# Optimization experiments

Measured on AMD Instinct MI355X. Metric: run time of the kernel, lower is better.

The kernel has to match this reference:

```python
import jax, jax.numpy as jnp
import numpy as np

SIGMA = 0.2
BN_EPS = 1e-5


def setup_inputs() -> dict:
    key = jax.random.key(0)
    k1, k2, k3, k4 = jax.random.split(key, 4)
    B, F, K, M = 8, 16384, 3, 64
    normals = jax.random.normal(k1, (B, 3, F), dtype=jnp.float32)
    # normalize to unit vectors (face normals), keeps math well-conditioned
    normals = normals / jnp.linalg.norm(normals, axis=1, keepdims=True)
    weight_alpha = jax.random.uniform(k2, (1, M, 4), dtype=jnp.float32) * np.pi
    weight_beta = jax.random.uniform(k3, (1, M, 4), dtype=jnp.float32) * 2 * np.pi
    bn_gamma = jnp.ones((M,), dtype=jnp.float32)
    bn_beta = jnp.zeros((M,), dtype=jnp.float32)
    neighbor_index = jax.random.randint(k4, (B, F, K), 0, F, dtype=jnp.int64)
    return {"normals": normals, "weight_alpha": weight_alpha,
            "weight_beta": weight_beta, "bn_gamma": bn_gamma,
            "bn_beta": bn_beta, "neighbor_index": neighbor_index}


def reference(normals, weight_alpha, weight_beta, bn_gamma, bn_beta, neighbor_index):
    # normals: [B, 3, F]; neighbor_index: [B, F, K]
    B, _, F = normals.shape
    K = neighbor_index.shape[-1]
    # kernel points on unit sphere from spherical angles: [3, M, 4]
    sa, ca = jnp.sin(weight_alpha), jnp.cos(weight_alpha)
    sb, cb = jnp.sin(weight_beta), jnp.cos(weight_beta)
    w = jnp.concatenate([sa * cb, sa * sb, ca], axis=0)  # [3, M, 4]

    nt = jnp.transpose(normals, (0, 2, 1))  # [B, F, 3]
    # gather neighbor normals per batch: [B, F, K, 3]
    neigh = jax.vmap(lambda n, idx: n[idx])(nt, neighbor_index)
    # points per face: center + K neighbors -> [B, F, K+1, 3]
    pts = jnp.concatenate([nt[:, :, None, :], neigh], axis=2)

    # squared distance via expansion: ||p||^2 + ||w||^2 - 2 p.w
    dot = jnp.einsum('bfic,cmj->bmfij', pts, w)        # [B, M, F, K+1, 4]
    p2 = jnp.sum(pts * pts, axis=-1)                   # [B, F, K+1]
    w2 = jnp.sum(w * w, axis=0)                        # [M, 4]
    dist = (p2[:, None, :, :, None] + w2[None, :, None, None, :] - 2.0 * dot)

    feat = jnp.sum(jnp.exp(dist / (-2.0 * SIGMA ** 2)), axis=(3, 4))
    feat = feat / float((K + 1) * 4)                   # [B, M, F]

    # BatchNorm1d (training-mode batch stats over B and F per channel M)
    mean = jnp.mean(feat, axis=(0, 2), keepdims=True)
    var = jnp.var(feat, axis=(0, 2), keepdims=True)
    xhat = (feat - mean) / jnp.sqrt(var + BN_EPS)
    out = xhat * bn_gamma[None, :, None] + bn_beta[None, :, None]
    return jax.nn.relu(out)
```

## Files before the change

kernel.cpp:

```cpp
#include <hip/hip_runtime.h>
#include <hip/hip_fp16.h>

#define B_DIM 8
#define F_DIM 16384
#define K_DIM 3
#define M_DIM 64
#define LOG2E 1.4426950408889634f

#define WS_Q   65536
#define WS_G   131072
#define WS_NEED ((size_t)WS_G * 4 + (size_t)B_DIM * F_DIM * M_DIM * 2)

#define FB_WS_Q 32768

__global__ __launch_bounds__(256) void fkc_g16_kernel(
    const float* __restrict__ normals,
    const float* __restrict__ walpha,
    const float* __restrict__ wbeta,
    __half* __restrict__ G)
{
    __shared__ float4 sW[256];
    const int tid = threadIdx.x;
    {
        float a = walpha[tid], b = wbeta[tid];
        float sa = sinf(a), ca = cosf(a);
        float sb = sinf(b), cb = cosf(b);
        float wx = sa * cb, wy = sa * sb, wz = ca;
        float w2 = wx * wx + wy * wy + wz * wz;
        sW[tid] = make_float4(wx * 25.0f * LOG2E, wy * 25.0f * LOG2E,
                              wz * 25.0f * LOG2E, -12.5f * LOG2E * (w2 + 1.0f));
    }
    __syncthreads();

    const int b  = blockIdx.x >> 8;
    const int fc = blockIdx.x & 255;
    const int fl = tid & 63, mq = tid >> 6;
    const int f  = (fc << 6) + fl;

    const float* nb = normals + (size_t)b * 3 * F_DIM;
    const float px = nb[f], py = nb[F_DIM + f], pz = nb[2 * F_DIM + f];

    union { __half2 h2[8]; float4 f4[2]; } u;
#pragma unroll
    for (int r = 0; r < 8; ++r) {
        float g[2];
#pragma unroll
        for (int c = 0; c < 2; ++c) {
            const int m = mq * 16 + r * 2 + c;
            float4 w0 = sW[m * 4 + 0], w1 = sW[m * 4 + 1];
            float4 w2 = sW[m * 4 + 2], w3 = sW[m * 4 + 3];
            float e0 = __builtin_amdgcn_exp2f(fmaf(w0.x, px, fmaf(w0.y, py, fmaf(w0.z, pz, w0.w))));
            float e1 = __builtin_amdgcn_exp2f(fmaf(w1.x, px, fmaf(w1.y, py, fmaf(w1.z, pz, w1.w))));
            float e2 = __builtin_amdgcn_exp2f(fmaf(w2.x, px, fmaf(w2.y, py, fmaf(w2.z, pz, w2.w))));
            float e3 = __builtin_amdgcn_exp2f(fmaf(w3.x, px, fmaf(w3.y, py, fmaf(w3.z, pz, w3.w))));
            g[c] = (e0 + e1) + (e2 + e3);
        }
        u.h2[r] = __floats2half2_rn(g[0], g[1]);
    }
    float4* dst = (float4*)(G + ((size_t)(b * F_DIM + f)) * M_DIM + mq * 16);
    dst[0] = u.f4[0];
    dst[1] = u.f4[1];
}

__global__ __launch_bounds__(256) void fkc_gath16_kernel(
    const __half* __restrict__ G,
    const int*   __restrict__ nidx,
    float* __restrict__ out,
    float* __restrict__ ws)
{
    __shared__ float T[2][128][34];
    const int tid = threadIdx.x;
    const int b  = blockIdx.x & 7;
    const int fc = blockIdx.x >> 3;
    const int fl = tid & 127, mh = tid >> 7;
    const int f  = (fc << 7) + fl;

    const int* ib = nidx + ((size_t)(b * F_DIM + f)) * K_DIM;
    const int i1 = ib[0], i2 = ib[1], i3 = ib[2];

    const size_t gb = (size_t)b * F_DIM * M_DIM + (size_t)mh * 32;
    const float4* r0 = (const float4*)(G + gb + (size_t)f  * M_DIM);
    const float4* r1 = (const float4*)(G + gb + (size_t)i1 * M_DIM);
    const float4* r2 = (const float4*)(G + gb + (size_t)i2 * M_DIM);
    const float4* r3 = (const float4*)(G + gb + (size_t)i3 * M_DIM);

    union F4H { float4 f4; __half2 h2[4]; };
    float v[32];
#pragma unroll
    for (int c = 0; c < 4; ++c) {
        F4H a, x, y, z, acc;
        a.f4 = r0[c]; x.f4 = r1[c]; y.f4 = r2[c]; z.f4 = r3[c];
#pragma unroll
        for (int k = 0; k < 4; ++k) {
            acc.h2[k] = __hadd2(__hadd2(a.h2[k], x.h2[k]), __hadd2(y.h2[k], z.h2[k]));
            float2 t = __half22float2(acc.h2[k]);
            v[c * 8 + k * 2]     = t.x;
            v[c * 8 + k * 2 + 1] = t.y;
        }
    }

    {
        float* ob = out + ((size_t)b * M_DIM + mh * 32) * F_DIM + f;
#pragma unroll
        for (int k = 0; k < 32; ++k) ob[(size_t)k * F_DIM] = v[k];
    }

#pragma unroll
    for (int k = 0; k < 32; ++k) T[mh][fl][k] = v[k];
    __syncthreads();
    {
        const int rmh = tid >> 7, rml = (tid >> 2) & 31, rfs = tid & 3;
        float s = 0.f, q = 0.f;
#pragma unroll
        for (int i = 0; i < 32; ++i) {
            float val = T[rmh][rfs * 32 + i][rml];
            s += val;
            q = fmaf(val, val, q);
        }
        s += __shfl_xor(s, 1, 64);  q += __shfl_xor(q, 1, 64);
        s += __shfl_xor(s, 2, 64);  q += __shfl_xor(q, 2, 64);
        if (rfs == 0) {
            int m = rmh * 32 + rml;
            int slot = m * 1024 + b * 128 + fc;
            ws[slot] = s;
            ws[WS_Q + slot] = q;
        }
    }
}

__global__ __launch_bounds__(256) void fkc_bn2_kernel(
    float* __restrict__ out,
    const float* __restrict__ gamma,
    const float* __restrict__ beta,
    const float* __restrict__ ws)
{
    __shared__ float sS[4], sQ[4];
    __shared__ float sAC[2];
    const int row = blockIdx.x;
    const int m = row & 63;
    const int tid = threadIdx.x;
    const int wave = tid >> 6, lane = tid & 63;

    {
        const float* p = ws + m * 1024;
        const float* r = ws + WS_Q + m * 1024;
        float s = (p[tid] + p[tid + 256]) + (p[tid + 512] + p[tid + 768]);
        float q = (r[tid] + r[tid + 256]) + (r[tid + 512] + r[tid + 768]);
#pragma unroll
        for (int off = 32; off >= 1; off >>= 1) {
            s += __shfl_xor(s, off, 64);
            q += __shfl_xor(q, off, 64);
        }
        if (lane == 0) { sS[wave] = s; sQ[wave] = q; }
    }
    __syncthreads();
    if (tid == 0) {
        float s = (sS[0] + sS[1]) + (sS[2] + sS[3]);
        float q = (sQ[0] + sQ[1]) + (sQ[2] + sQ[3]);
        const float invcnt = 1.0f / (float)(B_DIM * F_DIM);
        float meanS = s * invcnt;
        float meanF = meanS * (1.0f / 16.0f);
        float ef2   = q * invcnt * (1.0f / 256.0f);
        float var   = ef2 - meanF * meanF;
        float inv   = rsqrtf(var + 1e-5f);
        float A = gamma[m] * inv;
        sAC[0] = A * (1.0f / 16.0f);
        sAC[1] = beta[m] - meanF * A;
    }
    __syncthreads();

    const float A = sAC[0], C = sAC[1];
    float4* p4 = (float4*)(out + (size_t)row * F_DIM);
#pragma unroll
    for (int i = 0; i < 16; ++i) {
        float4 v = p4[tid + i * 256];
        v.x = fmaxf(fmaf(v.x, A, C), 0.0f);
        v.y = fmaxf(fmaf(v.y, A, C), 0.0f);
        v.z = fmaxf(fmaf(v.z, A, C), 0.0f);
        v.w = fmaxf(fmaf(v.w, A, C), 0.0f);
        p4[tid + i * 256] = v;
    }
}

__global__ __launch_bounds__(256) void fb_feat_kernel(
    const float* __restrict__ normals, const float* __restrict__ walpha,
    const float* __restrict__ wbeta, const int* __restrict__ nidx,
    float* __restrict__ feat_out, float* __restrict__ ws)
{
    __shared__ float4 sW[64];
    __shared__ float sRS[16][32], sRQ[16][32];
    const int tid = threadIdx.x;
    const int b  = blockIdx.x >> 8;
    const int mc = (blockIdx.x >> 6) & 3;
    const int fc = blockIdx.x & 63;
    if (tid < 64) {
        int idx = mc * 64 + tid;
        float a = walpha[idx], bb = wbeta[idx];
        float sa = sinf(a), ca = cosf(a);
        float sb = sinf(bb), cb = cosf(bb);
        float wx = sa * cb, wy = sa * sb, wz = ca;
        float w2 = wx * wx + wy * wy + wz * wz;
        sW[tid] = make_float4(wx * 25.0f * LOG2E, wy * 25.0f * LOG2E,
                              wz * 25.0f * LOG2E, -12.5f * LOG2E * (w2 + 1.0f));
    }
    __syncthreads();
    const int f = (fc << 8) + tid;
    const float* nb = normals + (size_t)b * 3 * F_DIM;
    float px[4], py[4], pz[4];
    px[0] = nb[f]; py[0] = nb[F_DIM + f]; pz[0] = nb[2 * F_DIM + f];
    const int* ib = nidx + ((size_t)b * F_DIM + f) * K_DIM;
#pragma unroll
    for (int k = 0; k < K_DIM; ++k) {
        int id = ib[k];
        px[k + 1] = nb[id]; py[k + 1] = nb[F_DIM + id]; pz[k + 1] = nb[2 * F_DIM + id];
    }
    const int wave = tid >> 6, lane = tid & 63;
    float* outb = feat_out + ((size_t)b * M_DIM + mc * 16) * F_DIM + f;
#pragma unroll 2
    for (int m = 0; m < 16; ++m) {
        float s0 = 0.f, s1 = 0.f, s2 = 0.f, s3 = 0.f;
#pragma unroll
        for (int j = 0; j < 4; ++j) {
            float4 w = sW[m * 4 + j];
            s0 += __builtin_amdgcn_exp2f(fmaf(w.x, px[0], fmaf(w.y, py[0], fmaf(w.z, pz[0], w.w))));
            s1 += __builtin_amdgcn_exp2f(fmaf(w.x, px[1], fmaf(w.y, py[1], fmaf(w.z, pz[1], w.w))));
            s2 += __builtin_amdgcn_exp2f(fmaf(w.x, px[2], fmaf(w.y, py[2], fmaf(w.z, pz[2], w.w))));
            s3 += __builtin_amdgcn_exp2f(fmaf(w.x, px[3], fmaf(w.y, py[3], fmaf(w.z, pz[3], w.w))));
        }
        float fv = ((s0 + s1) + (s2 + s3)) * (1.0f / 16.0f);
        outb[(size_t)m * F_DIM] = fv;
        float s = fv, q = fv * fv;
        s += __shfl_xor(s, 8, 64);  q += __shfl_xor(q, 8, 64);
        s += __shfl_xor(s, 16, 64); q += __shfl_xor(q, 16, 64);
        s += __shfl_xor(s, 32, 64); q += __shfl_xor(q, 32, 64);
        if (lane < 8) { sRS[m][wave * 8 + lane] = s; sRQ[m][wave * 8 + lane] = q; }
    }
    __syncthreads();
    {
        const int m = tid >> 4, j = tid & 15;
        float s = sRS[m][j] + sRS[m][j + 16];
        float q = sRQ[m][j] + sRQ[m][j + 16];
        s += __shfl_xor(s, 1, 64);  q += __shfl_xor(q, 1, 64);
        s += __shfl_xor(s, 2, 64);  q += __shfl_xor(q, 2, 64);
        s += __shfl_xor(s, 4, 64);  q += __shfl_xor(q, 4, 64);
        s += __shfl_xor(s, 8, 64);  q += __shfl_xor(q, 8, 64);
        if (j == 0) {
            int slot = (mc * 16 + m) * 512 + b * 64 + fc;
            ws[slot] = s;
            ws[FB_WS_Q + slot] = q;
        }
    }
}

__global__ __launch_bounds__(256) void fb_bn_kernel(
    float* __restrict__ out, const float* __restrict__ gamma,
    const float* __restrict__ beta, const float* __restrict__ ws)
{
    __shared__ float sS[4], sQ[4];
    __shared__ float sAC[2];
    const int row = blockIdx.x;
    const int m = row & 63;
    const int tid = threadIdx.x;
    const int wave = tid >> 6, lane = tid & 63;
    {
        float s = ws[m * 512 + tid]           + ws[m * 512 + tid + 256];
        float q = ws[FB_WS_Q + m * 512 + tid] + ws[FB_WS_Q + m * 512 + tid + 256];
#pragma unroll
        for (int off = 32; off >= 1; off >>= 1) {
            s += __shfl_xor(s, off, 64);
            q += __shfl_xor(q, off, 64);
        }
        if (lane == 0) { sS[wave] = s; sQ[wave] = q; }
    }
    __syncthreads();
    if (tid == 0) {
        float s = (sS[0] + sS[1]) + (sS[2] + sS[3]);
        float q = (sQ[0] + sQ[1]) + (sQ[2] + sQ[3]);
        const float invcnt = 1.0f / (float)(B_DIM * F_DIM);
        float mean = s * invcnt;
        float var  = q * invcnt - mean * mean;
        float inv  = rsqrtf(var + 1e-5f);
        float A = gamma[m] * inv;
        sAC[0] = A;
        sAC[1] = beta[m] - mean * A;
    }
    __syncthreads();
    const float A = sAC[0], C = sAC[1];
    float4* p4 = (float4*)(out + (size_t)row * F_DIM);
#pragma unroll
    for (int i = 0; i < 16; ++i) {
        float4 v = p4[tid + i * 256];
        v.x = fmaxf(fmaf(v.x, A, C), 0.0f);
        v.y = fmaxf(fmaf(v.y, A, C), 0.0f);
        v.z = fmaxf(fmaf(v.z, A, C), 0.0f);
        v.w = fmaxf(fmaf(v.w, A, C), 0.0f);
        p4[tid + i * 256] = v;
    }
}

extern "C" void kernel_launch(void* const* d_in, const int* in_sizes, int n_in,
                              void* d_out, int out_size, void* d_ws, size_t ws_size,
                              hipStream_t stream)
{
    const float* normals = (const float*)d_in[0];
    const float* walpha  = (const float*)d_in[1];
    const float* wbeta   = (const float*)d_in[2];
    const float* gamma   = (const float*)d_in[3];
    const float* beta    = (const float*)d_in[4];
    const int*   nidx    = (const int*)d_in[5];
    float* out = (float*)d_out;
    float* ws  = (float*)d_ws;

    if (ws_size >= WS_NEED) {
        __half* G = (__half*)(ws + WS_G);
        hipLaunchKernelGGL(fkc_g16_kernel, dim3(2048), dim3(256), 0, stream,
                           normals, walpha, wbeta, G);
        hipLaunchKernelGGL(fkc_gath16_kernel, dim3(1024), dim3(256), 0, stream,
                           G, nidx, out, ws);
        hipLaunchKernelGGL(fkc_bn2_kernel, dim3(B_DIM * M_DIM), dim3(256), 0, stream,
                           out, gamma, beta, ws);
    } else {
        hipLaunchKernelGGL(fb_feat_kernel, dim3(2048), dim3(256), 0, stream,
                           normals, walpha, wbeta, nidx, out, ws);
        hipLaunchKernelGGL(fb_bn_kernel, dim3(B_DIM * M_DIM), dim3(256), 0, stream,
                           out, gamma, beta, ws);
    }
}
```

Before: 47.20 us.

## Stage G writes through LDS for coalesced stores; shrink gather LDS to half2

The G-producing kernel now stages each block's 64x64 half tile in shared memory and writes it back as contiguous float4 rows, so global stores are fully coalesced instead of strided per-thread row chunks. The gather kernel stores its per-face sums to a half2 LDS tile instead of float, halving shared memory use, adds a launch-bounds occupancy hint of 8 blocks, and streams output writes inside the load loop instead of holding 32 floats in registers. The cost is an extra LDS round trip and barrier in the first kernel and half-precision unpacking in the statistics reduction.

```diff
diff --git a/kernel.cpp b/kernel.cpp
--- a/kernel.cpp
+++ b/kernel.cpp
@@ -20,6 +20,7 @@
     __half* __restrict__ G)
 {
     __shared__ float4 sW[256];
+    __shared__ __half Gt[64][68];
     const int tid = threadIdx.x;
     {
         float a = walpha[tid], b = wbeta[tid];
@@ -40,7 +41,7 @@
     const float* nb = normals + (size_t)b * 3 * F_DIM;
     const float px = nb[f], py = nb[F_DIM + f], pz = nb[2 * F_DIM + f];
 
-    union { __half2 h2[8]; float4 f4[2]; } u;
+    union { __half2 h2[8]; float2 f2[4]; } u;
 #pragma unroll
     for (int r = 0; r < 8; ++r) {
         float g[2];
@@ -57,18 +58,30 @@
         }
         u.h2[r] = __floats2half2_rn(g[0], g[1]);
     }
-    float4* dst = (float4*)(G + ((size_t)(b * F_DIM + f)) * M_DIM + mq * 16);
-    dst[0] = u.f4[0];
-    dst[1] = u.f4[1];
-}
-
-__global__ __launch_bounds__(256) void fkc_gath16_kernel(
+#pragma unroll
+    for (int c = 0; c < 4; ++c)
+        *(float2*)&Gt[fl][mq * 16 + c * 4] = u.f2[c];
+    __syncthreads();
+
+    {
+        const int r = tid >> 2, c0 = (tid & 3) * 16;
+        float2 w0 = *(float2*)&Gt[r][c0 + 0];
+        float2 w1 = *(float2*)&Gt[r][c0 + 4];
+        float2 w2 = *(float2*)&Gt[r][c0 + 8];
+        float2 w3 = *(float2*)&Gt[r][c0 + 12];
+        float4* dst = (float4*)(G + ((size_t)b * F_DIM + (fc << 6)) * M_DIM);
+        dst[tid * 2 + 0] = make_float4(w0.x, w0.y, w1.x, w1.y);
+        dst[tid * 2 + 1] = make_float4(w2.x, w2.y, w3.x, w3.y);
+    }
+}
+
+__global__ __launch_bounds__(256, 8) void fkc_gath16_kernel(
     const __half* __restrict__ G,
     const int*   __restrict__ nidx,
     float* __restrict__ out,
     float* __restrict__ ws)
 {
-    __shared__ float T[2][128][34];
+    __shared__ __half2 T2[2][128][18];
     const int tid = threadIdx.x;
     const int b  = blockIdx.x & 7;
     const int fc = blockIdx.x >> 3;
@@ -85,35 +98,31 @@
     const float4* r3 = (const float4*)(G + gb + (size_t)i3 * M_DIM);
 
     union F4H { float4 f4; __half2 h2[4]; };
-    float v[32];
+    float* ob = out + ((size_t)b * M_DIM + mh * 32) * F_DIM + f;
 #pragma unroll
     for (int c = 0; c < 4; ++c) {
-        F4H a, x, y, z, acc;
+        F4H a, x, y, z;
         a.f4 = r0[c]; x.f4 = r1[c]; y.f4 = r2[c]; z.f4 = r3[c];
+        union { __half2 h2[4]; float2 f2[2]; } hh;
 #pragma unroll
         for (int k = 0; k < 4; ++k) {
-            acc.h2[k] = __hadd2(__hadd2(a.h2[k], x.h2[k]), __hadd2(y.h2[k], z.h2[k]));
-            float2 t = __half22float2(acc.h2[k]);
-            v[c * 8 + k * 2]     = t.x;
-            v[c * 8 + k * 2 + 1] = t.y;
-        }
-    }
-
-    {
-        float* ob = out + ((size_t)b * M_DIM + mh * 32) * F_DIM + f;
-#pragma unroll
-        for (int k = 0; k < 32; ++k) ob[(size_t)k * F_DIM] = v[k];
-    }
-
-#pragma unroll
-    for (int k = 0; k < 32; ++k) T[mh][fl][k] = v[k];
-    __syncthreads();
+            hh.h2[k] = __hadd2(__hadd2(a.h2[k], x.h2[k]), __hadd2(y.h2[k], z.h2[k]));
+            float2 t = __half22float2(hh.h2[k]);
+            ob[(size_t)(c * 8 + k * 2)     * F_DIM] = t.x;
+            ob[(size_t)(c * 8 + k * 2 + 1) * F_DIM] = t.y;
+        }
+        *(float2*)&T2[mh][fl][c * 4 + 0] = hh.f2[0];
+        *(float2*)&T2[mh][fl][c * 4 + 2] = hh.f2[1];
+    }
+    __syncthreads();
+
     {
         const int rmh = tid >> 7, rml = (tid >> 2) & 31, rfs = tid & 3;
         float s = 0.f, q = 0.f;
 #pragma unroll
         for (int i = 0; i < 32; ++i) {
-            float val = T[rmh][rfs * 32 + i][rml];
+            __half2 p = T2[rmh][rfs * 32 + i][rml >> 1];
+            float val = (rml & 1) ? __high2float(p) : __low2float(p);
             s += val;
             q = fmaf(val, val, q);
         }
```

New measurement: 48.28 us (median of 2 runs). +2.3%, slower.

## Stage gathered features as fp16 tiles and write final output once in BN kernel

Applied to the files above, without the earlier changes.

The gather kernel no longer writes fp32 features to the output and re-reads them in the BN pass. It now writes fp16 tiles, already transposed through LDS, to workspace, and the BN kernel reads those tiles and writes the normalized fp32 output once. The aim is to cut the fp32 write plus read-modify-write round trip, roughly halving intermediate traffic. The G kernel's block order is also interleaved by batch. This needs more workspace and rounds the features to fp16 once more.

```diff
diff --git a/kernel.cpp b/kernel.cpp
--- a/kernel.cpp
+++ b/kernel.cpp
@@ -9,7 +9,8 @@
 
 #define WS_Q   65536
 #define WS_G   131072
-#define WS_NEED ((size_t)WS_G * 4 + (size_t)B_DIM * F_DIM * M_DIM * 2)
+#define WS_T   4325376
+#define WS_NEED ((size_t)34078720)
 
 #define FB_WS_Q 32768
 
@@ -32,8 +33,8 @@
     }
     __syncthreads();
 
-    const int b  = blockIdx.x >> 8;
-    const int fc = blockIdx.x & 255;
+    const int b  = blockIdx.x & 7;
+    const int fc = blockIdx.x >> 3;
     const int fl = tid & 63, mq = tid >> 6;
     const int f  = (fc << 6) + fl;
 
@@ -57,7 +58,7 @@
         }
         u.h2[r] = __floats2half2_rn(g[0], g[1]);
     }
-    float4* dst = (float4*)(G + ((size_t)(b * F_DIM + f)) * M_DIM + mq * 16);
+    float4* dst = (float4*)(G + ((size_t)b * F_DIM + f) * M_DIM + mq * 16);
     dst[0] = u.f4[0];
     dst[1] = u.f4[1];
 }
@@ -65,7 +66,7 @@
 __global__ __launch_bounds__(256) void fkc_gath16_kernel(
     const __half* __restrict__ G,
     const int*   __restrict__ nidx,
-    float* __restrict__ out,
+    __half* __restrict__ tiles,
     float* __restrict__ ws)
 {
     __shared__ float T[2][128][34];
@@ -85,38 +86,36 @@
     const float4* r3 = (const float4*)(G + gb + (size_t)i3 * M_DIM);
 
     union F4H { float4 f4; __half2 h2[4]; };
-    float v[32];
 #pragma unroll
     for (int c = 0; c < 4; ++c) {
-        F4H a, x, y, z, acc;
+        F4H a, x, y, z;
         a.f4 = r0[c]; x.f4 = r1[c]; y.f4 = r2[c]; z.f4 = r3[c];
 #pragma unroll
         for (int k = 0; k < 4; ++k) {
-            acc.h2[k] = __hadd2(__hadd2(a.h2[k], x.h2[k]), __hadd2(y.h2[k], z.h2[k]));
-            float2 t = __half22float2(acc.h2[k]);
-            v[c * 8 + k * 2]     = t.x;
-            v[c * 8 + k * 2 + 1] = t.y;
-        }
-    }
-
-    {
-        float* ob = out + ((size_t)b * M_DIM + mh * 32) * F_DIM + f;
-#pragma unroll
-        for (int k = 0; k < 32; ++k) ob[(size_t)k * F_DIM] = v[k];
-    }
-
-#pragma unroll
-    for (int k = 0; k < 32; ++k) T[mh][fl][k] = v[k];
-    __syncthreads();
+            __half2 hs = __hadd2(__hadd2(a.h2[k], x.h2[k]), __hadd2(y.h2[k], z.h2[k]));
+            float2 t = __half22float2(hs);
+            T[mh][fl][c * 8 + k * 2]     = t.x;
+            T[mh][fl][c * 8 + k * 2 + 1] = t.y;
+        }
+    }
+    __syncthreads();
+
     {
         const int rmh = tid >> 7, rml = (tid >> 2) & 31, rfs = tid & 3;
         float s = 0.f, q = 0.f;
-#pragma unroll
-        for (int i = 0; i < 32; ++i) {
-            float val = T[rmh][rfs * 32 + i][rml];
-            s += val;
-            q = fmaf(val, val, q);
-        }
+        union { __half2 h2[16]; float4 f4[4]; } pk;
+#pragma unroll
+        for (int i = 0; i < 32; i += 2) {
+            float v0 = T[rmh][rfs * 32 + i][rml];
+            float v1 = T[rmh][rfs * 32 + i + 1][rml];
+            s += v0 + v1;
+            q = fmaf(v0, v0, fmaf(v1, v1, q));
+            pk.h2[i >> 1] = __floats2half2_rn(v0, v1);
+        }
+        float4* td = (float4*)(tiles + ((size_t)(b * 128 + fc)) * 8192
+                               + (size_t)rmh * 4096 + rml * 128 + rfs * 32);
+        td[0] = pk.f4[0]; td[1] = pk.f4[1]; td[2] = pk.f4[2]; td[3] = pk.f4[3];
+
         s += __shfl_xor(s, 1, 64);  q += __shfl_xor(q, 1, 64);
         s += __shfl_xor(s, 2, 64);  q += __shfl_xor(q, 2, 64);
         if (rfs == 0) {
@@ -128,16 +127,17 @@
     }
 }
 
-__global__ __launch_bounds__(256) void fkc_bn2_kernel(
+__global__ __launch_bounds__(256) void fkc_bnf_kernel(
     float* __restrict__ out,
+    const __half* __restrict__ tiles,
     const float* __restrict__ gamma,
     const float* __restrict__ beta,
     const float* __restrict__ ws)
 {
     __shared__ float sS[4], sQ[4];
     __shared__ float sAC[2];
-    const int row = blockIdx.x;
-    const int m = row & 63;
+    const int b = blockIdx.x & 7;
+    const int m = blockIdx.x >> 3;
     const int tid = threadIdx.x;
     const int wave = tid >> 6, lane = tid & 63;
 
@@ -170,15 +170,30 @@
     __syncthreads();
 
     const float A = sAC[0], C = sAC[1];
-    float4* p4 = (float4*)(out + (size_t)row * F_DIM);
-#pragma unroll
-    for (int i = 0; i < 16; ++i) {
-        float4 v = p4[tid + i * 256];
-        v.x = fmaxf(fmaf(v.x, A, C), 0.0f);
-        v.y = fmaxf(fmaf(v.y, A, C), 0.0f);
-        v.z = fmaxf(fmaf(v.z, A, C), 0.0f);
-        v.w = fmaxf(fmaf(v.w, A, C), 0.0f);
-        p4[tid + i * 256] = v;
+    const int fc = tid >> 1, sub = tid & 1;
+    const float4* t4 = (const float4*)(tiles + ((size_t)(b * 128 + fc)) * 8192
+                       + (size_t)(m >> 5) * 4096 + (m & 31) * 128 + sub * 64);
+    float4* op = (float4*)(out + ((size_t)(b * M_DIM + m)) * F_DIM
+                           + (size_t)fc * 128 + sub * 64);
+#pragma unroll
+    for (int k = 0; k < 8; ++k) {
+        union { float4 f4; __half2 h2[4]; } u;
+        u.f4 = t4[k];
+        float2 p0 = __half22float2(u.h2[0]);
+        float2 p1 = __half22float2(u.h2[1]);
+        float2 p2 = __half22float2(u.h2[2]);
+        float2 p3 = __half22float2(u.h2[3]);
+        float4 o0, o1;
+        o0.x = fmaxf(fmaf(p0.x, A, C), 0.0f);
+        o0.y = fmaxf(fmaf(p0.y, A, C), 0.0f);
+        o0.z = fmaxf(fmaf(p1.x, A, C), 0.0f);
+        o0.w = fmaxf(fmaf(p1.y, A, C), 0.0f);
+        o1.x = fmaxf(fmaf(p2.x, A, C), 0.0f);
+        o1.y = fmaxf(fmaf(p2.y, A, C), 0.0f);
+        o1.z = fmaxf(fmaf(p3.x, A, C), 0.0f);
+        o1.w = fmaxf(fmaf(p3.y, A, C), 0.0f);
+        op[k * 2 + 0] = o0;
+        op[k * 2 + 1] = o1;
     }
 }
 
@@ -312,13 +327,14 @@
     float* ws  = (float*)d_ws;
 
     if (ws_size >= WS_NEED) {
-        __half* G = (__half*)(ws + WS_G);
+        __half* G     = (__half*)(ws + WS_G);
+        __half* tiles = (__half*)(ws + WS_T);
         hipLaunchKernelGGL(fkc_g16_kernel, dim3(2048), dim3(256), 0, stream,
                            normals, walpha, wbeta, G);
         hipLaunchKernelGGL(fkc_gath16_kernel, dim3(1024), dim3(256), 0, stream,
-                           G, nidx, out, ws);
-        hipLaunchKernelGGL(fkc_bn2_kernel, dim3(B_DIM * M_DIM), dim3(256), 0, stream,
-                           out, gamma, beta, ws);
+                           G, nidx, tiles, ws);
+        hipLaunchKernelGGL(fkc_bnf_kernel, dim3(512), dim3(256), 0, stream,
+                           out, tiles, gamma, beta, ws);
     } else {
         hipLaunchKernelGGL(fb_feat_kernel, dim3(2048), dim3(256), 0, stream,
                            normals, walpha, wbeta, nidx, out, ws);
```

Result: slower. 51.84 us (+9.8%).
